# Performance work log

Hardware: AMD Instinct MI355X
Metric: run time of the kernel (lower is better)

## Reference

```python
import jax, jax.numpy as jnp
import numpy as np

N, E, D, G, S, H = 100000, 1600000, 64, 1024, 4096, 128
BN_EPS = 1e-5


def setup_inputs() -> dict:
    key = jax.random.key(0)
    ks = jax.random.split(key, 24)
    x = jax.random.normal(ks[0], (N, D), jnp.float32)
    sid = jax.random.randint(ks[1], (N,), 0, S)
    x = x.at[:, 5].set(sid.astype(jnp.float32))  # column 5 holds integer substructure ids
    edge_index = jax.random.randint(ks[2], (2, E), 0, N, dtype=jnp.int32)
    batch = jnp.sort(jax.random.randint(ks[3], (N,), 0, G, dtype=jnp.int32))

    def lin(k, fan_in, shape):
        return jax.random.normal(k, shape, jnp.float32) / np.sqrt(fan_in)

    return {
        "x": x, "edge_index": edge_index, "batch": batch,
        # substructure attention net: Linear(D,64) -> tanh -> Linear(64,1,no bias)
        "w1": lin(ks[4], D, (D, 64)), "b1": jnp.zeros((64,), jnp.float32),
        "w2": lin(ks[5], 64, (64,)),
        "cw0": lin(ks[6], D + 1, (D + 1, H)), "cb0": jnp.zeros((H,), jnp.float32),
        "cw_rest": lin(ks[7], H, (3, H, H)), "cb_rest": jnp.zeros((3, H), jnp.float32),
        # BatchNorm1d (eval mode: running stats)
        "bn_gamma": jnp.ones((4, H), jnp.float32), "bn_beta": jnp.zeros((4, H), jnp.float32),
        "bn_mean": 0.1 * jax.random.normal(ks[8], (4, H), jnp.float32),
        "bn_var": jax.random.uniform(ks[9], (4, H), jnp.float32, 0.5, 1.5),
        # pred head: Linear(128,64) -> ELU -> Linear(64,1)
        "hw1": lin(ks[10], H, (H, 64)), "hb1": jnp.zeros((64,), jnp.float32),
        "hw2": lin(ks[11], 64, (64, 1)), "hb2": jnp.zeros((1,), jnp.float32),
    }


def _subst_attention(x, subst_ids, w1, b1, w2):
    ones = jnp.ones((x.shape[0],), x.dtype)
    cnt = jax.ops.segment_sum(ones, subst_ids, num_segments=S)
    sums = jax.ops.segment_sum(x, subst_ids, num_segments=S)
    means = sums / jnp.maximum(cnt, 1.0)[:, None]          # [S, D] per-substructure mean
    scores = jnp.tanh(means @ w1 + b1) @ w2                # [S]
    attn = jax.nn.softmax(scores, axis=0)                  # softmax over substructures
    return attn[subst_ids][:, None]                        # [N, 1] broadcast back to atoms


def _gcn(x, W, b, row, col, norm, n):
    h = x @ W                                              # [N, H]
    msg = h[row] * norm[:, None]                           # gather + scale  [E+N, H]
    return jax.ops.segment_sum(msg, col, num_segments=n) + b


def reference(x, edge_index, batch, w1, b1, w2, cw0, cb0, cw_rest, cb_rest,
              bn_gamma, bn_beta, bn_mean, bn_var, hw1, hb1, hw2, hb2):
    n = x.shape[0]
    subst_ids = jax.lax.stop_gradient(x[:, 5]).astype(jnp.int32)
    attn = _subst_attention(x, subst_ids, w1, b1, w2)
    h = jnp.concatenate([x, attn], axis=1)                 # [N, D+1]

    # add self loops, symmetric GCN normalization (as in PyG GCNConv)
    loops = jnp.arange(n, dtype=edge_index.dtype)
    row = jnp.concatenate([edge_index[0], loops])
    col = jnp.concatenate([edge_index[1], loops])
    deg = jax.ops.segment_sum(jnp.ones_like(row, dtype=h.dtype), col, num_segments=n)
    dinv = jax.lax.rsqrt(jnp.maximum(deg, 1.0))
    norm = dinv[row] * dinv[col]

    def bn(z, i):
        return (z - bn_mean[i]) * jax.lax.rsqrt(bn_var[i] + BN_EPS) * bn_gamma[i] + bn_beta[i]

    h = jax.nn.elu(bn(_gcn(h, cw0, cb0, row, col, norm, n), 0))
    for i in range(3):
        z = bn(_gcn(h, cw_rest[i], cb_rest[i], row, col, norm, n), i + 1)
        h = jax.nn.elu(z) if i < 2 else jax.nn.relu(z)

    # global mean pool over graphs
    gcnt = jax.ops.segment_sum(jnp.ones((n,), h.dtype), batch, num_segments=G)
    pooled = jax.ops.segment_sum(h, batch, num_segments=G) / jnp.maximum(gcnt, 1.0)[:, None]

    return jax.nn.elu(pooled @ hw1 + hb1) @ hw2 + hb2      # [G, 1]
```

## Files before the change

kernel.cpp:

```cpp
#include <hip/hip_runtime.h>
#include <math.h>

static constexpr int SS = 4096;
static constexpr int HH = 128;
static constexpr float EPS_BN = 1e-5f;

typedef __attribute__((ext_vector_type(8))) short bf16x8;
typedef __attribute__((ext_vector_type(4))) float f32x4;

__device__ inline unsigned short f2bf(float f) {
  unsigned int u = __float_as_uint(f);
  return (unsigned short)((u + 0x7fffu + ((u >> 16) & 1u)) >> 16);
}
__device__ inline float bflo(unsigned int u) { return __uint_as_float(u << 16); }
__device__ inline float bfhi(unsigned int u) { return __uint_as_float(u & 0xffff0000u); }


__device__ void wpack_body(const float* __restrict__ W, unsigned short* __restrict__ out,
                           int nkc, int idx) {
  if (idx >= 8 * nkc * 64) return;
  int lane = idx & 63;
  int kc = (idx >> 6) % nkc;
  int nt = idx / (64 * nkc);
  int colc = nt * 16 + (lane & 15);
  int k0 = kc * 32 + (lane >> 4) * 8;
  unsigned int w[4];
  #pragma unroll
  for (int i = 0; i < 4; ++i) {
    unsigned short a = f2bf(W[(size_t)(k0 + 2 * i) * 128 + colc]);
    unsigned short b = f2bf(W[(size_t)(k0 + 2 * i + 1) * 128 + colc]);
    w[i] = (unsigned int)a | ((unsigned int)b << 16);
  }
  *(uint4*)&out[(size_t)idx * 8] = make_uint4(w[0], w[1], w[2], w[3]);
}

__global__ __launch_bounds__(256)
void gcn_front1(const int* __restrict__ col, int* __restrict__ fill, int* __restrict__ pos,
                const float* __restrict__ x, float* __restrict__ cnt, float* __restrict__ sums,
                unsigned int* __restrict__ xh, const int* __restrict__ batch,
                int* __restrict__ gstart,
                const float* __restrict__ cw0, const float* __restrict__ cwr,
                unsigned short* __restrict__ wpk0, unsigned short* __restrict__ wpkr,
                const float* __restrict__ cb0, const float* __restrict__ cbr,
                const float* __restrict__ bng, const float* __restrict__ bnb,
                const float* __restrict__ bnm, const float* __restrict__ bnv,
                float* __restrict__ bnS, float* __restrict__ bnT,
                int n, int e, int G,
                int nbPos, int nbSub, int nbXb, int nbGb, int nbW0, int nbWr) {
  int b = blockIdx.x;
  int t = threadIdx.x;
  if (b < nbPos) {
    int i = b * 256 + t;
    if (i < e) pos[i] = atomicAdd(&fill[col[i]], 1);
    return;
  }
  b -= nbPos;
  if (b < nbSub) {
    int node = b * 4 + (t >> 6);
    int lane = t & 63;
    if (node >= n) return;
    const float* xr = x + (size_t)node * 64;
    float v = xr[lane];
    int sid = (int)__shfl(v, 5, 64);
    if (lane == 0) atomicAdd(&cnt[sid], 1.0f);
    atomicAdd(&sums[(size_t)sid * 64 + lane], v);
    return;
  }
  b -= nbSub;
  if (b < nbXb) {
    int i = b * 256 + t;
    if (i >= n * 32) return;
    int pr = i & 31;
    float2 v = *(const float2*)&x[(size_t)(i >> 5) * 64 + pr * 2];
    if (pr == 2) v.y = 0.f;
    xh[i] = (unsigned int)f2bf(v.x) | ((unsigned int)f2bf(v.y) << 16);
    return;
  }
  b -= nbXb;
  if (b < nbGb) {
    int g = b * 256 + t;
    if (g > G) return;
    if (g == G) { gstart[G] = n; return; }
    int lo = 0, hi = n;
    while (lo < hi) { int mid = (lo + hi) >> 1; if (batch[mid] < g) lo = mid + 1; else hi = mid; }
    gstart[g] = lo;
    return;
  }
  b -= nbGb;
  if (b < nbW0) { wpack_body(cw0, wpk0, 2, b * 256 + t); return; }
  b -= nbW0;
  if (b < 3 * nbWr) {
    int l = b / nbWr, bb = b % nbWr;
    wpack_body(cwr + (size_t)l * HH * HH, wpkr + (size_t)l * 8 * 4 * 64 * 8, 4, bb * 256 + t);
    return;
  }
  b -= 3 * nbWr;
  {
    int i = b * 256 + t;
    if (i >= 512) return;
    int l = i >> 7, c = i & 127;
    float S = rsqrtf(bnv[i] + EPS_BN) * bng[i];
    float bias = (l == 0) ? cb0[c] : cbr[(l - 1) * 128 + c];
    bnS[i] = S;
    bnT[i] = fmaf(bias - bnm[i], S, bnb[i]);
  }
}


__global__ void gcn_scores(const float* __restrict__ sums, const float* __restrict__ cnt,
                           const float* __restrict__ w1, const float* __restrict__ b1,
                           const float* __restrict__ w2, float* __restrict__ scores) {
  int s = blockIdx.x * 4 + (threadIdx.x >> 6);
  int j = threadIdx.x & 63;
  float r = 1.0f / fmaxf(cnt[s], 1.0f);
  const float* ss = sums + (size_t)s * 64;
  float acc = b1[j];
  #pragma unroll 8
  for (int d = 0; d < 64; ++d) acc = fmaf(ss[d] * r, w1[d * 64 + j], acc);
  float t = tanhf(acc) * w2[j];
  #pragma unroll
  for (int off = 32; off; off >>= 1) t += __shfl_down(t, off, 64);
  if (j == 0) scores[s] = t;
}

__global__ void gcn_softmax(float* __restrict__ sc) {
  int t = threadIdx.x;
  int wid = t >> 6;
  float v[4]; float m = -INFINITY;
  for (int i = 0; i < 4; ++i) { v[i] = sc[t + i * 1024]; m = fmaxf(m, v[i]); }
  for (int off = 32; off; off >>= 1) m = fmaxf(m, __shfl_xor(m, off, 64));
  __shared__ float wmax[16];
  if ((t & 63) == 0) wmax[wid] = m;
  __syncthreads();
  if (t == 0) { float mm = wmax[0]; for (int i = 1; i < 16; ++i) mm = fmaxf(mm, wmax[i]); wmax[0] = mm; }
  __syncthreads();
  float M = wmax[0];
  float s = 0.f;
  for (int i = 0; i < 4; ++i) { v[i] = expf(v[i] - M); s += v[i]; }
  for (int off = 32; off; off >>= 1) s += __shfl_xor(s, off, 64);
  __shared__ float wsum[16];
  if ((t & 63) == 0) wsum[wid] = s;
  __syncthreads();
  if (t == 0) { float ts = 0.f; for (int i = 0; i < 16; ++i) ts += wsum[i]; wsum[0] = ts; }
  __syncthreads();
  float inv = 1.0f / wsum[0];
  for (int i = 0; i < 4; ++i) sc[t + i * 1024] = v[i] * inv;
}


__global__ void gcn_scan1(const int* __restrict__ fill, int* __restrict__ rowstart,
                          int* __restrict__ bsum, float* __restrict__ dinv, int n) {
  __shared__ int tmp[1024];
  int t = threadIdx.x; int g = blockIdx.x * 1024 + t;
  int v = (g < n) ? fill[g] : 0;
  if (g < n) dinv[g] = rsqrtf((float)v + 1.0f);
  tmp[t] = v; __syncthreads();
  for (int off = 1; off < 1024; off <<= 1) {
    int a = (t >= off) ? tmp[t - off] : 0; __syncthreads();
    tmp[t] += a; __syncthreads();
  }
  if (g < n) rowstart[g] = tmp[t] - v;
  if (t == 1023) bsum[blockIdx.x] = tmp[t];
}

__global__ void gcn_scan2(int* __restrict__ bsum, int nb) {
  __shared__ int tmp[128];
  int t = threadIdx.x;
  int v = (t < nb) ? bsum[t] : 0;
  tmp[t] = v; __syncthreads();
  for (int off = 1; off < 128; off <<= 1) {
    int a = (t >= off) ? tmp[t - off] : 0; __syncthreads();
    tmp[t] += a; __syncthreads();
  }
  if (t < nb) bsum[t] = tmp[t] - v;
}

__global__ void gcn_scan3(int* __restrict__ rowstart, const int* __restrict__ bsum, int n, int e) {
  int g = blockIdx.x * 1024 + threadIdx.x;
  if (g < n) rowstart[g] += bsum[blockIdx.x];
  if (g == 0) rowstart[n] = e;
}


__global__ __launch_bounds__(256)
void gcn_front3(const float* __restrict__ x, const float* __restrict__ attn,
                float2* __restrict__ np,
                const int* __restrict__ row, const int* __restrict__ col,
                const int* __restrict__ pos, const int* __restrict__ rowstart,
                const float* __restrict__ dinv, int2* __restrict__ sedge,
                int n, int e, int nbNp) {
  int b = blockIdx.x;
  int t = threadIdx.x;
  if (b < nbNp) {
    int i = b * 256 + t;
    if (i >= n) return;
    int sid = (int)x[(size_t)i * 64 + 5];
    np[i] = make_float2((float)sid, attn[sid]);
    return;
  }
  b -= nbNp;
  int i = b * 256 + t;
  if (i >= e) return;
  int c = col[i], r = row[i];
  sedge[rowstart[c] + pos[i]] = make_int2(r, __float_as_int(dinv[r] * dinv[c]));
}


__global__ __launch_bounds__(256)
void gcn_front4(const unsigned int* __restrict__ xh, const float2* __restrict__ np,
                const int2* __restrict__ sedge, const int* __restrict__ rowstart,
                const float* __restrict__ dinv,
                unsigned int* __restrict__ s0b, float* __restrict__ s0x,
                int n, int nbAx) {
  int blk = blockIdx.x;
  int t = threadIdx.x;
  if (blk < nbAx) {
    int node = blk * 4 + (t >> 6);
    int lane = t & 63;
    if (node >= n) return;
    int g = lane >> 3, sl = lane & 7;
    float di = dinv[node], d2 = di * di;
    const uint4* x4 = (const uint4*)xh;
    float a[8];
    if (g == 0) {
      uint4 u = x4[(size_t)node * 8 + sl];
      a[0] = bflo(u.x) * d2; a[1] = bfhi(u.x) * d2;
      a[2] = bflo(u.y) * d2; a[3] = bfhi(u.y) * d2;
      a[4] = bflo(u.z) * d2; a[5] = bfhi(u.z) * d2;
      a[6] = bflo(u.w) * d2; a[7] = bfhi(u.w) * d2;
    } else {
      #pragma unroll
      for (int i = 0; i < 8; ++i) a[i] = 0.f;
    }
    int s_ = rowstart[node], e_ = rowstart[node + 1];
    for (int b = s_; b < e_; b += 8) {
      int idx = b + (lane & 7);
      int2 se = (idx < e_) ? sedge[idx] : make_int2(node, 0);
      int src = __shfl(se.x, g, 8);
      float w = __int_as_float(__shfl(se.y, g, 8));
      uint4 u = x4[(size_t)src * 8 + sl];
      a[0] = fmaf(bflo(u.x), w, a[0]); a[1] = fmaf(bfhi(u.x), w, a[1]);
      a[2] = fmaf(bflo(u.y), w, a[2]); a[3] = fmaf(bfhi(u.y), w, a[3]);
      a[4] = fmaf(bflo(u.z), w, a[4]); a[5] = fmaf(bfhi(u.z), w, a[5]);
      a[6] = fmaf(bflo(u.w), w, a[6]); a[7] = fmaf(bfhi(u.w), w, a[7]);
    }
    #pragma unroll
    for (int i = 0; i < 8; ++i) {
      a[i] += __shfl_xor(a[i], 8, 64);
      a[i] += __shfl_xor(a[i], 16, 64);
      a[i] += __shfl_xor(a[i], 32, 64);
    }
    if (g == 0) {
      uint4 o;
      o.x = (unsigned)f2bf(a[0]) | ((unsigned)f2bf(a[1]) << 16);
      o.y = (unsigned)f2bf(a[2]) | ((unsigned)f2bf(a[3]) << 16);
      o.z = (unsigned)f2bf(a[4]) | ((unsigned)f2bf(a[5]) << 16);
      o.w = (unsigned)f2bf(a[6]) | ((unsigned)f2bf(a[7]) << 16);
      ((uint4*)s0b)[(size_t)node * 8 + sl] = o;
    }
    return;
  }
  int i = (blk - nbAx) * 256 + t;
  if (i >= n) return;
  float di = dinv[i], d2 = di * di;
  float2 self = np[i];
  float a5 = d2 * self.x, a64 = d2 * self.y;
  int s_ = rowstart[i], e_ = rowstart[i + 1];
  for (int ee = s_; ee < e_; ++ee) {
    int2 se = sedge[ee];
    float w = __int_as_float(se.y);
    float2 v = np[se.x];
    a5 = fmaf(v.x, w, a5);
    a64 = fmaf(v.y, w, a64);
  }
  s0x[(size_t)i * 2] = a5;
  s0x[(size_t)i * 2 + 1] = a64;
}


__global__ __launch_bounds__(256)
void gcn_aggB(const unsigned short* __restrict__ hB, const int2* __restrict__ sedge,
              const int* __restrict__ rowstart, const float* __restrict__ dinv,
              unsigned int* __restrict__ sBb, int n) {
  int node = blockIdx.x * 4 + (threadIdx.x >> 6);
  int lane = threadIdx.x & 63;
  if (node >= n) return;
  int g = lane >> 4, sl = lane & 15;
  float di = dinv[node], d2 = di * di;
  const uint4* h4 = (const uint4*)hB;
  float a[8];
  if (g == 0) {
    uint4 u = h4[(size_t)node * 16 + sl];
    a[0] = bflo(u.x) * d2; a[1] = bfhi(u.x) * d2;
    a[2] = bflo(u.y) * d2; a[3] = bfhi(u.y) * d2;
    a[4] = bflo(u.z) * d2; a[5] = bfhi(u.z) * d2;
    a[6] = bflo(u.w) * d2; a[7] = bfhi(u.w) * d2;
  } else {
    #pragma unroll
    for (int i = 0; i < 8; ++i) a[i] = 0.f;
  }
  int s_ = rowstart[node], e_ = rowstart[node + 1];
  for (int b = s_; b < e_; b += 8) {
    int idx = b + (lane & 7);
    int2 se = (idx < e_) ? sedge[idx] : make_int2(node, 0);
    #pragma unroll
    for (int j = 0; j < 2; ++j) {
      int src = __shfl(se.x, j * 4 + g, 8);
      float w = __int_as_float(__shfl(se.y, j * 4 + g, 8));
      uint4 u = h4[(size_t)src * 16 + sl];
      a[0] = fmaf(bflo(u.x), w, a[0]); a[1] = fmaf(bfhi(u.x), w, a[1]);
      a[2] = fmaf(bflo(u.y), w, a[2]); a[3] = fmaf(bfhi(u.y), w, a[3]);
      a[4] = fmaf(bflo(u.z), w, a[4]); a[5] = fmaf(bfhi(u.z), w, a[5]);
      a[6] = fmaf(bflo(u.w), w, a[6]); a[7] = fmaf(bfhi(u.w), w, a[7]);
    }
  }
  #pragma unroll
  for (int i = 0; i < 8; ++i) {
    a[i] += __shfl_xor(a[i], 16, 64);
    a[i] += __shfl_xor(a[i], 32, 64);
  }
  if (g == 0) {
    uint4 o;
    o.x = (unsigned)f2bf(a[0]) | ((unsigned)f2bf(a[1]) << 16);
    o.y = (unsigned)f2bf(a[2]) | ((unsigned)f2bf(a[3]) << 16);
    o.z = (unsigned)f2bf(a[4]) | ((unsigned)f2bf(a[5]) << 16);
    o.w = (unsigned)f2bf(a[6]) | ((unsigned)f2bf(a[7]) << 16);
    ((uint4*)sBb)[(size_t)node * 16 + sl] = o;
  }
}


__global__ __launch_bounds__(256)
void gcn_mm_mfma(const unsigned short* __restrict__ A, const unsigned short* __restrict__ Wpk,
                 const float* __restrict__ bnS, const float* __restrict__ bnT,
                 unsigned short* __restrict__ hB, int relu) {
  __shared__ unsigned short tile[4][16][136];
  int t = threadIdx.x;
  int wid = t >> 6, l = t & 63;
  int rowA = l & 15, kg = l >> 4;
  size_t row0w = (size_t)blockIdx.x * 64 + wid * 16;
  const unsigned short* Ar = A + (row0w + rowA) * 128 + kg * 8;
  bf16x8 af[4];
  #pragma unroll
  for (int kc = 0; kc < 4; ++kc) af[kc] = *(const bf16x8*)(Ar + kc * 32);
  f32x4 acc[8];
  #pragma unroll
  for (int nt = 0; nt < 8; ++nt) acc[nt] = (f32x4){0.f, 0.f, 0.f, 0.f};
  const unsigned short* wp = Wpk + (size_t)l * 8;
  #pragma unroll
  for (int kc = 0; kc < 4; ++kc) {
    bf16x8 bf[8];
    #pragma unroll
    for (int nt = 0; nt < 8; ++nt)
      bf[nt] = *(const bf16x8*)(wp + (size_t)(nt * 4 + kc) * 512);
    #pragma unroll
    for (int nt = 0; nt < 8; ++nt)
      acc[nt] = __builtin_amdgcn_mfma_f32_16x16x32_bf16(af[kc], bf[nt], acc[nt], 0, 0, 0);
  }
  int colb = l & 15, rb = kg * 4;
  #pragma unroll
  for (int nt = 0; nt < 8; ++nt) {
    int c = nt * 16 + colb;
    float S = bnS[c], T = bnT[c];
    #pragma unroll
    for (int j = 0; j < 4; ++j) {
      float v = fmaf(acc[nt][j], S, T);
      v = relu ? fmaxf(v, 0.f) : (v > 0.f ? v : expf(v) - 1.f);
      tile[wid][rb + j][c] = f2bf(v);
    }
  }
  __syncthreads();
  #pragma unroll
  for (int i = 0; i < 4; ++i) {
    int m = i * 64 + l;
    int row = m >> 4, chunk = m & 15;
    uint4 v = *(const uint4*)&tile[wid][row][chunk * 8];
    *(uint4*)&hB[(row0w + row) * 128 + chunk * 8] = v;
  }
}

__global__ __launch_bounds__(256)
void gcn_mm0_mfma(const unsigned short* __restrict__ A, const float* __restrict__ s0x,
                  const unsigned short* __restrict__ Wpk0, const float* __restrict__ cw0,
                  const float* __restrict__ bnS, const float* __restrict__ bnT,
                  unsigned short* __restrict__ hB) {
  __shared__ unsigned short tile[4][16][136];
  int t = threadIdx.x;
  int wid = t >> 6, l = t & 63;
  int rowA = l & 15, kg = l >> 4;
  size_t row0w = (size_t)blockIdx.x * 64 + wid * 16;
  const unsigned short* Ar = A + (row0w + rowA) * 64 + kg * 8;
  bf16x8 af[2];
  #pragma unroll
  for (int kc = 0; kc < 2; ++kc) af[kc] = *(const bf16x8*)(Ar + kc * 32);
  f32x4 acc[8];
  #pragma unroll
  for (int nt = 0; nt < 8; ++nt) acc[nt] = (f32x4){0.f, 0.f, 0.f, 0.f};
  const unsigned short* wp = Wpk0 + (size_t)l * 8;
  #pragma unroll
  for (int kc = 0; kc < 2; ++kc) {
    bf16x8 bf[8];
    #pragma unroll
    for (int nt = 0; nt < 8; ++nt)
      bf[nt] = *(const bf16x8*)(wp + (size_t)(nt * 2 + kc) * 512);
    #pragma unroll
    for (int nt = 0; nt < 8; ++nt)
      acc[nt] = __builtin_amdgcn_mfma_f32_16x16x32_bf16(af[kc], bf[nt], acc[nt], 0, 0, 0);
  }
  int colb = l & 15, rb = kg * 4;
  float2 ax[4];
  #pragma unroll
  for (int j = 0; j < 4; ++j) ax[j] = *(const float2*)&s0x[(row0w + rb + j) * 2];
  #pragma unroll
  for (int nt = 0; nt < 8; ++nt) {
    int c = nt * 16 + colb;
    float w5 = cw0[5 * 128 + c], w64 = cw0[64 * 128 + c];
    float S = bnS[c], T = bnT[c];
    #pragma unroll
    for (int j = 0; j < 4; ++j) {
      float z = acc[nt][j] + ax[j].x * w5 + ax[j].y * w64;
      float v = fmaf(z, S, T);
      v = v > 0.f ? v : expf(v) - 1.f;
      tile[wid][rb + j][c] = f2bf(v);
    }
  }
  __syncthreads();
  #pragma unroll
  for (int i = 0; i < 4; ++i) {
    int m = i * 64 + l;
    int row = m >> 4, chunk = m & 15;
    uint4 v = *(const uint4*)&tile[wid][row][chunk * 8];
    *(uint4*)&hB[(row0w + row) * 128 + chunk * 8] = v;
  }
}


__global__ void gcn_pool2(const unsigned short* __restrict__ hB, const int* __restrict__ gstart,
                          float* __restrict__ pooled, int G) {
  int g = blockIdx.x * 4 + (threadIdx.x >> 6);
  int lane = threadIdx.x & 63;
  if (g >= G) return;
  int s = gstart[g], epos = gstart[g + 1];
  const unsigned int* h32 = (const unsigned int*)hB;
  float ax = 0.f, ay = 0.f;
  for (int i = s; i < epos; ++i) {
    unsigned int u = h32[(size_t)i * 64 + lane];
    ax += bflo(u);
    ay += bfhi(u);
  }
  float r = 1.0f / fmaxf((float)(epos - s), 1.0f);
  ((float2*)pooled)[(size_t)g * 64 + lane] = make_float2(ax * r, ay * r);
}

__global__ void gcn_head(const float* __restrict__ pooled,
                         const float* __restrict__ hw1, const float* __restrict__ hb1,
                         const float* __restrict__ hw2, const float* __restrict__ hb2,
                         float* __restrict__ out, int g) {
  int gi = blockIdx.x * 4 + (threadIdx.x >> 6);
  int j = threadIdx.x & 63;
  if (gi >= g) return;
  const float* p = pooled + (size_t)gi * 128;
  float acc = hb1[j];
  #pragma unroll 8
  for (int k = 0; k < 128; ++k) acc = fmaf(p[k], hw1[k * 64 + j], acc);
  float t = acc > 0.f ? acc : expf(acc) - 1.f;
  t *= hw2[j];
  #pragma unroll
  for (int off = 32; off; off >>= 1) t += __shfl_down(t, off, 64);
  if (j == 0) out[gi] = t + hb2[0];
}


extern "C" void kernel_launch(void* const* d_in, const int* in_sizes, int n_in,
                              void* d_out, int out_size, void* d_ws, size_t ws_size,
                              hipStream_t stream) {
  const float* x   = (const float*)d_in[0];
  const int*   ei  = (const int*)d_in[1];
  const int*   batch = (const int*)d_in[2];
  const float* w1  = (const float*)d_in[3];
  const float* b1  = (const float*)d_in[4];
  const float* w2  = (const float*)d_in[5];
  const float* cw0 = (const float*)d_in[6];
  const float* cb0 = (const float*)d_in[7];
  const float* cwr = (const float*)d_in[8];
  const float* cbr = (const float*)d_in[9];
  const float* bng = (const float*)d_in[10];
  const float* bnb = (const float*)d_in[11];
  const float* bnm = (const float*)d_in[12];
  const float* bnv = (const float*)d_in[13];
  const float* hw1 = (const float*)d_in[14];
  const float* hb1 = (const float*)d_in[15];
  const float* hw2 = (const float*)d_in[16];
  const float* hb2 = (const float*)d_in[17];
  float* out = (float*)d_out;
  (void)n_in; (void)ws_size;

  const int n = in_sizes[0] / 64;
  const int e = in_sizes[1] / 2;
  const int G = out_size;
  const int* row = ei;
  const int* col = ei + e;
  const int nb128 = (n + 127) / 128;
  const int n_pad = nb128 * 128;

  char* p = (char*)d_ws;
  auto take = [&](size_t bytes) { char* r = p; p += (bytes + 255) & ~(size_t)255; return r; };
  float* cnt    = (float*)take((size_t)SS * 4);
  float* sums   = (float*)take((size_t)SS * 64 * 4);
  float* attn   = (float*)take((size_t)SS * 4);
  float* dinv   = (float*)take((size_t)n * 4);
  int*   rowst  = (int*)take(((size_t)n + 1) * 4);
  int*   fill   = (int*)take((size_t)n * 4);
  int*   pos    = (int*)take((size_t)e * 4);
  int*   bsum   = (int*)take(128 * 4);
  int*   gstart = (int*)take(((size_t)G + 1) * 4);
  int2*  sedge  = (int2*)take((size_t)e * 8);
  float* pooled = (float*)take((size_t)G * HH * 4);
  float2* np    = (float2*)take((size_t)n * 8);
  unsigned int* xh = (unsigned int*)take((size_t)n * 32 * 4);
  unsigned int* s0b = (unsigned int*)take((size_t)n_pad * 32 * 4);
  float* s0x    = (float*)take((size_t)n_pad * 2 * 4);
  unsigned int* sBb = (unsigned int*)take((size_t)n_pad * 64 * 4);
  unsigned short* hB = (unsigned short*)take((size_t)n_pad * HH * 2);
  unsigned short* wpk0 = (unsigned short*)take((size_t)8 * 2 * 64 * 8 * 2);
  unsigned short* wpkr = (unsigned short*)take((size_t)3 * 8 * 4 * 64 * 8 * 2);
  float* bnS    = (float*)take(4 * 128 * 4);
  float* bnT    = (float*)take(4 * 128 * 4);

  hipMemsetAsync(cnt, 0, (size_t)SS * 4, stream);
  hipMemsetAsync(sums, 0, (size_t)SS * 64 * 4, stream);
  hipMemsetAsync(fill, 0, (size_t)n * 4, stream);

  int nbPos = (e + 255) / 256;
  int nbSub = (n + 3) / 4;
  int nbXb  = (n * 32 + 255) / 256;
  int nbGb  = (G + 1 + 255) / 256;
  int nbW0 = 4, nbWr = 8, nbBnp = 2;
  int front1 = nbPos + nbSub + nbXb + nbGb + nbW0 + 3 * nbWr + nbBnp;
  gcn_front1<<<front1, 256, 0, stream>>>(col, fill, pos, x, cnt, sums, xh, batch, gstart,
      cw0, cwr, wpk0, wpkr, cb0, cbr, bng, bnb, bnm, bnv, bnS, bnT,
      n, e, G, nbPos, nbSub, nbXb, nbGb, nbW0, nbWr);

  gcn_scores<<<SS / 4, 256, 0, stream>>>(sums, cnt, w1, b1, w2, attn);
  gcn_softmax<<<1, 1024, 0, stream>>>(attn);

  int nb = (n + 1023) / 1024;
  gcn_scan1<<<nb, 1024, 0, stream>>>(fill, rowst, bsum, dinv, n);
  gcn_scan2<<<1, 128, 0, stream>>>(bsum, nb);
  gcn_scan3<<<nb, 1024, 0, stream>>>(rowst, bsum, n, e);

  int nbNp = (n + 255) / 256, nbSc = (e + 255) / 256;
  gcn_front3<<<nbNp + nbSc, 256, 0, stream>>>(x, attn, np, row, col, pos, rowst, dinv,
      sedge, n, e, nbNp);

  int nbAx = (n + 3) / 4, nbAnp = (n + 255) / 256;
  gcn_front4<<<nbAx + nbAnp, 256, 0, stream>>>(xh, np, sedge, rowst, dinv, s0b, s0x, n, nbAx);
  gcn_mm0_mfma<<<n_pad / 64, 256, 0, stream>>>((const unsigned short*)s0b, s0x, wpk0, cw0,
      bnS, bnT, hB);

  for (int l = 0; l < 3; ++l) {
    gcn_aggB<<<(n + 3) / 4, 256, 0, stream>>>(hB, sedge, rowst, dinv, sBb, n);
    gcn_mm_mfma<<<n_pad / 64, 256, 0, stream>>>((const unsigned short*)sBb,
        wpkr + (size_t)l * 8 * 4 * 64 * 8, bnS + (l + 1) * 128, bnT + (l + 1) * 128,
        hB, l == 2 ? 1 : 0);
  }

  gcn_pool2<<<(G + 3) / 4, 256, 0, stream>>>(hB, gstart, pooled, G);
  gcn_head<<<(G + 3) / 4, 256, 0, stream>>>(pooled, hw1, hb1, hw2, hb2, out, G);
}
```

Baseline: 634.6 us.

## Fuse neighbor aggregation into MFMA matmul kernels for each GCN layer

```diff
diff --git a/kernel.cpp b/kernel.cpp
--- a/kernel.cpp
+++ b/kernel.cpp
@@ -207,142 +207,56 @@
 
 
 __global__ __launch_bounds__(256)
-void gcn_front4(const unsigned int* __restrict__ xh, const float2* __restrict__ np,
-                const int2* __restrict__ sedge, const int* __restrict__ rowstart,
-                const float* __restrict__ dinv,
-                unsigned int* __restrict__ s0b, float* __restrict__ s0x,
-                int n, int nbAx) {
-  int blk = blockIdx.x;
-  int t = threadIdx.x;
-  if (blk < nbAx) {
-    int node = blk * 4 + (t >> 6);
-    int lane = t & 63;
-    if (node >= n) return;
-    int g = lane >> 3, sl = lane & 7;
-    float di = dinv[node], d2 = di * di;
-    const uint4* x4 = (const uint4*)xh;
-    float a[8];
-    if (g == 0) {
-      uint4 u = x4[(size_t)node * 8 + sl];
-      a[0] = bflo(u.x) * d2; a[1] = bfhi(u.x) * d2;
-      a[2] = bflo(u.y) * d2; a[3] = bfhi(u.y) * d2;
-      a[4] = bflo(u.z) * d2; a[5] = bfhi(u.z) * d2;
-      a[6] = bflo(u.w) * d2; a[7] = bfhi(u.w) * d2;
-    } else {
-      #pragma unroll
-      for (int i = 0; i < 8; ++i) a[i] = 0.f;
-    }
-    int s_ = rowstart[node], e_ = rowstart[node + 1];
-    for (int b = s_; b < e_; b += 8) {
-      int idx = b + (lane & 7);
-      int2 se = (idx < e_) ? sedge[idx] : make_int2(node, 0);
-      int src = __shfl(se.x, g, 8);
-      float w = __int_as_float(__shfl(se.y, g, 8));
-      uint4 u = x4[(size_t)src * 8 + sl];
-      a[0] = fmaf(bflo(u.x), w, a[0]); a[1] = fmaf(bfhi(u.x), w, a[1]);
-      a[2] = fmaf(bflo(u.y), w, a[2]); a[3] = fmaf(bfhi(u.y), w, a[3]);
-      a[4] = fmaf(bflo(u.z), w, a[4]); a[5] = fmaf(bfhi(u.z), w, a[5]);
-      a[6] = fmaf(bflo(u.w), w, a[6]); a[7] = fmaf(bfhi(u.w), w, a[7]);
-    }
-    #pragma unroll
-    for (int i = 0; i < 8; ++i) {
-      a[i] += __shfl_xor(a[i], 8, 64);
-      a[i] += __shfl_xor(a[i], 16, 64);
-      a[i] += __shfl_xor(a[i], 32, 64);
-    }
-    if (g == 0) {
-      uint4 o;
-      o.x = (unsigned)f2bf(a[0]) | ((unsigned)f2bf(a[1]) << 16);
-      o.y = (unsigned)f2bf(a[2]) | ((unsigned)f2bf(a[3]) << 16);
-      o.z = (unsigned)f2bf(a[4]) | ((unsigned)f2bf(a[5]) << 16);
-      o.w = (unsigned)f2bf(a[6]) | ((unsigned)f2bf(a[7]) << 16);
-      ((uint4*)s0b)[(size_t)node * 8 + sl] = o;
-    }
-    return;
-  }
-  int i = (blk - nbAx) * 256 + t;
-  if (i >= n) return;
-  float di = dinv[i], d2 = di * di;
-  float2 self = np[i];
-  float a5 = d2 * self.x, a64 = d2 * self.y;
-  int s_ = rowstart[i], e_ = rowstart[i + 1];
-  for (int ee = s_; ee < e_; ++ee) {
-    int2 se = sedge[ee];
-    float w = __int_as_float(se.y);
-    float2 v = np[se.x];
-    a5 = fmaf(v.x, w, a5);
-    a64 = fmaf(v.y, w, a64);
-  }
-  s0x[(size_t)i * 2] = a5;
-  s0x[(size_t)i * 2 + 1] = a64;
-}
-
-
-__global__ __launch_bounds__(256)
-void gcn_aggB(const unsigned short* __restrict__ hB, const int2* __restrict__ sedge,
-              const int* __restrict__ rowstart, const float* __restrict__ dinv,
-              unsigned int* __restrict__ sBb, int n) {
-  int node = blockIdx.x * 4 + (threadIdx.x >> 6);
-  int lane = threadIdx.x & 63;
-  if (node >= n) return;
-  int g = lane >> 4, sl = lane & 15;
-  float di = dinv[node], d2 = di * di;
-  const uint4* h4 = (const uint4*)hB;
-  float a[8];
-  if (g == 0) {
-    uint4 u = h4[(size_t)node * 16 + sl];
-    a[0] = bflo(u.x) * d2; a[1] = bfhi(u.x) * d2;
-    a[2] = bflo(u.y) * d2; a[3] = bfhi(u.y) * d2;
-    a[4] = bflo(u.z) * d2; a[5] = bfhi(u.z) * d2;
-    a[6] = bflo(u.w) * d2; a[7] = bfhi(u.w) * d2;
-  } else {
-    #pragma unroll
-    for (int i = 0; i < 8; ++i) a[i] = 0.f;
-  }
-  int s_ = rowstart[node], e_ = rowstart[node + 1];
-  for (int b = s_; b < e_; b += 8) {
-    int idx = b + (lane & 7);
-    int2 se = (idx < e_) ? sedge[idx] : make_int2(node, 0);
-    #pragma unroll
-    for (int j = 0; j < 2; ++j) {
-      int src = __shfl(se.x, j * 4 + g, 8);
-      float w = __int_as_float(__shfl(se.y, j * 4 + g, 8));
-      uint4 u = h4[(size_t)src * 16 + sl];
-      a[0] = fmaf(bflo(u.x), w, a[0]); a[1] = fmaf(bfhi(u.x), w, a[1]);
-      a[2] = fmaf(bflo(u.y), w, a[2]); a[3] = fmaf(bfhi(u.y), w, a[3]);
-      a[4] = fmaf(bflo(u.z), w, a[4]); a[5] = fmaf(bfhi(u.z), w, a[5]);
-      a[6] = fmaf(bflo(u.w), w, a[6]); a[7] = fmaf(bfhi(u.w), w, a[7]);
-    }
-  }
-  #pragma unroll
-  for (int i = 0; i < 8; ++i) {
-    a[i] += __shfl_xor(a[i], 16, 64);
-    a[i] += __shfl_xor(a[i], 32, 64);
-  }
-  if (g == 0) {
-    uint4 o;
-    o.x = (unsigned)f2bf(a[0]) | ((unsigned)f2bf(a[1]) << 16);
-    o.y = (unsigned)f2bf(a[2]) | ((unsigned)f2bf(a[3]) << 16);
-    o.z = (unsigned)f2bf(a[4]) | ((unsigned)f2bf(a[5]) << 16);
-    o.w = (unsigned)f2bf(a[6]) | ((unsigned)f2bf(a[7]) << 16);
-    ((uint4*)sBb)[(size_t)node * 16 + sl] = o;
-  }
-}
-
-
-__global__ __launch_bounds__(256)
-void gcn_mm_mfma(const unsigned short* __restrict__ A, const unsigned short* __restrict__ Wpk,
+void gcn_layer_f(const unsigned short* __restrict__ hIn, const int2* __restrict__ sedge,
+                 const int* __restrict__ rowstart, const float* __restrict__ dinv,
+                 const unsigned short* __restrict__ Wpk,
                  const float* __restrict__ bnS, const float* __restrict__ bnT,
-                 unsigned short* __restrict__ hB, int relu) {
+                 unsigned short* __restrict__ hOut, int relu, int n) {
   __shared__ unsigned short tile[4][16][136];
   int t = threadIdx.x;
   int wid = t >> 6, l = t & 63;
-  int rowA = l & 15, kg = l >> 4;
+  int r = l & 15, kg = l >> 4;
   size_t row0w = (size_t)blockIdx.x * 64 + wid * 16;
-  const unsigned short* Ar = A + (row0w + rowA) * 128 + kg * 8;
+  int noderaw = (int)row0w + r;
+  bool valid = noderaw < n;
+  int node = valid ? noderaw : n - 1;
+  float di = dinv[node], d2 = di * di;
+  const uint4* h4 = (const uint4*)hIn;
+  float a[4][8];
+  #pragma unroll
+  for (int kc = 0; kc < 4; ++kc) {
+    uint4 u = h4[(size_t)node * 16 + kc * 4 + kg];
+    a[kc][0] = bflo(u.x) * d2; a[kc][1] = bfhi(u.x) * d2;
+    a[kc][2] = bflo(u.y) * d2; a[kc][3] = bfhi(u.y) * d2;
+    a[kc][4] = bflo(u.z) * d2; a[kc][5] = bfhi(u.z) * d2;
+    a[kc][6] = bflo(u.w) * d2; a[kc][7] = bfhi(u.w) * d2;
+  }
+  int s_ = valid ? rowstart[node] : 0;
+  int e_ = valid ? rowstart[node + 1] : 0;
+  int2 se = (s_ < e_) ? sedge[s_] : make_int2(0, 0);
+  for (int j = s_; j < e_; ++j) {
+    int2 cur = se;
+    if (j + 1 < e_) se = sedge[j + 1];
+    float w = __int_as_float(cur.y);
+    #pragma unroll
+    for (int kc = 0; kc < 4; ++kc) {
+      uint4 u = h4[(size_t)cur.x * 16 + kc * 4 + kg];
+      a[kc][0] = fmaf(bflo(u.x), w, a[kc][0]); a[kc][1] = fmaf(bfhi(u.x), w, a[kc][1]);
+      a[kc][2] = fmaf(bflo(u.y), w, a[kc][2]); a[kc][3] = fmaf(bfhi(u.y), w, a[kc][3]);
+      a[kc][4] = fmaf(bflo(u.z), w, a[kc][4]); a[kc][5] = fmaf(bfhi(u.z), w, a[kc][5]);
+      a[kc][6] = fmaf(bflo(u.w), w, a[kc][6]); a[kc][7] = fmaf(bfhi(u.w), w, a[kc][7]);
+    }
+  }
   bf16x8 af[4];
   #pragma unroll
-  for (int kc = 0; kc < 4; ++kc) af[kc] = *(const bf16x8*)(Ar + kc * 32);
+  for (int kc = 0; kc < 4; ++kc) {
+    uint4 pk;
+    pk.x = (unsigned)f2bf(a[kc][0]) | ((unsigned)f2bf(a[kc][1]) << 16);
+    pk.y = (unsigned)f2bf(a[kc][2]) | ((unsigned)f2bf(a[kc][3]) << 16);
+    pk.z = (unsigned)f2bf(a[kc][4]) | ((unsigned)f2bf(a[kc][5]) << 16);
+    pk.w = (unsigned)f2bf(a[kc][6]) | ((unsigned)f2bf(a[kc][7]) << 16);
+    af[kc] = *(bf16x8*)&pk;
+  }
   f32x4 acc[8];
   #pragma unroll
   for (int nt = 0; nt < 8; ++nt) acc[nt] = (f32x4){0.f, 0.f, 0.f, 0.f};
@@ -373,26 +287,72 @@
   #pragma unroll
   for (int i = 0; i < 4; ++i) {
     int m = i * 64 + l;
-    int row = m >> 4, chunk = m & 15;
-    uint4 v = *(const uint4*)&tile[wid][row][chunk * 8];
-    *(uint4*)&hB[(row0w + row) * 128 + chunk * 8] = v;
-  }
-}
+    int rr = m >> 4, chunk = m & 15;
+    uint4 v = *(const uint4*)&tile[wid][rr][chunk * 8];
+    *(uint4*)&hOut[(row0w + rr) * 128 + chunk * 8] = v;
+  }
+}
+
 
 __global__ __launch_bounds__(256)
-void gcn_mm0_mfma(const unsigned short* __restrict__ A, const float* __restrict__ s0x,
-                  const unsigned short* __restrict__ Wpk0, const float* __restrict__ cw0,
+void gcn_layer0_f(const unsigned int* __restrict__ xh, const float2* __restrict__ np,
+                  const int2* __restrict__ sedge, const int* __restrict__ rowstart,
+                  const float* __restrict__ dinv, const unsigned short* __restrict__ Wpk0,
+                  const float* __restrict__ cw0,
                   const float* __restrict__ bnS, const float* __restrict__ bnT,
-                  unsigned short* __restrict__ hB) {
+                  unsigned short* __restrict__ hOut, int n) {
   __shared__ unsigned short tile[4][16][136];
   int t = threadIdx.x;
   int wid = t >> 6, l = t & 63;
-  int rowA = l & 15, kg = l >> 4;
+  int r = l & 15, kg = l >> 4;
   size_t row0w = (size_t)blockIdx.x * 64 + wid * 16;
-  const unsigned short* Ar = A + (row0w + rowA) * 64 + kg * 8;
+  int noderaw = (int)row0w + r;
+  bool valid = noderaw < n;
+  int node = valid ? noderaw : n - 1;
+  float di = dinv[node], d2 = di * di;
+  const uint4* x4 = (const uint4*)xh;
+  float a[2][8];
+  #pragma unroll
+  for (int kc = 0; kc < 2; ++kc) {
+    uint4 u = x4[(size_t)node * 8 + kc * 4 + kg];
+    a[kc][0] = bflo(u.x) * d2; a[kc][1] = bfhi(u.x) * d2;
+    a[kc][2] = bflo(u.y) * d2; a[kc][3] = bfhi(u.y) * d2;
+    a[kc][4] = bflo(u.z) * d2; a[kc][5] = bfhi(u.z) * d2;
+    a[kc][6] = bflo(u.w) * d2; a[kc][7] = bfhi(u.w) * d2;
+  }
+  float a5 = 0.f, a64 = 0.f;
+  if (kg == 0) { float2 v = np[node]; a5 = d2 * v.x; a64 = d2 * v.y; }
+  int s_ = valid ? rowstart[node] : 0;
+  int e_ = valid ? rowstart[node + 1] : 0;
+  int2 se = (s_ < e_) ? sedge[s_] : make_int2(0, 0);
+  for (int j = s_; j < e_; ++j) {
+    int2 cur = se;
+    if (j + 1 < e_) se = sedge[j + 1];
+    float w = __int_as_float(cur.y);
+    #pragma unroll
+    for (int kc = 0; kc < 2; ++kc) {
+      uint4 u = x4[(size_t)cur.x * 8 + kc * 4 + kg];
+      a[kc][0] = fmaf(bflo(u.x), w, a[kc][0]); a[kc][1] = fmaf(bfhi(u.x), w, a[kc][1]);
+      a[kc][2] = fmaf(bflo(u.y), w, a[kc][2]); a[kc][3] = fmaf(bfhi(u.y), w, a[kc][3]);
+      a[kc][4] = fmaf(bflo(u.z), w, a[kc][4]); a[kc][5] = fmaf(bfhi(u.z), w, a[kc][5]);
+      a[kc][6] = fmaf(bflo(u.w), w, a[kc][6]); a[kc][7] = fmaf(bfhi(u.w), w, a[kc][7]);
+    }
+    if (kg == 0) {
+      float2 v = np[cur.x];
+      a5 = fmaf(v.x, w, a5);
+      a64 = fmaf(v.y, w, a64);
+    }
+  }
   bf16x8 af[2];
   #pragma unroll
-  for (int kc = 0; kc < 2; ++kc) af[kc] = *(const bf16x8*)(Ar + kc * 32);
+  for (int kc = 0; kc < 2; ++kc) {
+    uint4 pk;
+    pk.x = (unsigned)f2bf(a[kc][0]) | ((unsigned)f2bf(a[kc][1]) << 16);
+    pk.y = (unsigned)f2bf(a[kc][2]) | ((unsigned)f2bf(a[kc][3]) << 16);
+    pk.z = (unsigned)f2bf(a[kc][4]) | ((unsigned)f2bf(a[kc][5]) << 16);
+    pk.w = (unsigned)f2bf(a[kc][6]) | ((unsigned)f2bf(a[kc][7]) << 16);
+    af[kc] = *(bf16x8*)&pk;
+  }
   f32x4 acc[8];
   #pragma unroll
   for (int nt = 0; nt < 8; ++nt) acc[nt] = (f32x4){0.f, 0.f, 0.f, 0.f};
@@ -410,7 +370,10 @@
   int colb = l & 15, rb = kg * 4;
   float2 ax[4];
   #pragma unroll
-  for (int j = 0; j < 4; ++j) ax[j] = *(const float2*)&s0x[(row0w + rb + j) * 2];
+  for (int j = 0; j < 4; ++j) {
+    ax[j].x = __shfl(a5, rb + j, 64);
+    ax[j].y = __shfl(a64, rb + j, 64);
+  }
   #pragma unroll
   for (int nt = 0; nt < 8; ++nt) {
     int c = nt * 16 + colb;
@@ -428,9 +391,9 @@
   #pragma unroll
   for (int i = 0; i < 4; ++i) {
     int m = i * 64 + l;
-    int row = m >> 4, chunk = m & 15;
-    uint4 v = *(const uint4*)&tile[wid][row][chunk * 8];
-    *(uint4*)&hB[(row0w + row) * 128 + chunk * 8] = v;
+    int rr = m >> 4, chunk = m & 15;
+    uint4 v = *(const uint4*)&tile[wid][rr][chunk * 8];
+    *(uint4*)&hOut[(row0w + rr) * 128 + chunk * 8] = v;
   }
 }
 
@@ -518,10 +481,8 @@
   float* pooled = (float*)take((size_t)G * HH * 4);
   float2* np    = (float2*)take((size_t)n * 8);
   unsigned int* xh = (unsigned int*)take((size_t)n * 32 * 4);
-  unsigned int* s0b = (unsigned int*)take((size_t)n_pad * 32 * 4);
-  float* s0x    = (float*)take((size_t)n_pad * 2 * 4);
-  unsigned int* sBb = (unsigned int*)take((size_t)n_pad * 64 * 4);
-  unsigned short* hB = (unsigned short*)take((size_t)n_pad * HH * 2);
+  unsigned short* hP0 = (unsigned short*)take((size_t)n_pad * HH * 2);
+  unsigned short* hP1 = (unsigned short*)take((size_t)n_pad * HH * 2);
   unsigned short* wpk0 = (unsigned short*)take((size_t)8 * 2 * 64 * 8 * 2);
   unsigned short* wpkr = (unsigned short*)take((size_t)3 * 8 * 4 * 64 * 8 * 2);
   float* bnS    = (float*)take(4 * 128 * 4);
@@ -553,18 +514,15 @@
   gcn_front3<<<nbNp + nbSc, 256, 0, stream>>>(x, attn, np, row, col, pos, rowst, dinv,
       sedge, n, e, nbNp);
 
-  int nbAx = (n + 3) / 4, nbAnp = (n + 255) / 256;
-  gcn_front4<<<nbAx + nbAnp, 256, 0, stream>>>(xh, np, sedge, rowst, dinv, s0b, s0x, n, nbAx);
-  gcn_mm0_mfma<<<n_pad / 64, 256, 0, stream>>>((const unsigned short*)s0b, s0x, wpk0, cw0,
-      bnS, bnT, hB);
-
-  for (int l = 0; l < 3; ++l) {
-    gcn_aggB<<<(n + 3) / 4, 256, 0, stream>>>(hB, sedge, rowst, dinv, sBb, n);
-    gcn_mm_mfma<<<n_pad / 64, 256, 0, stream>>>((const unsigned short*)sBb,
-        wpkr + (size_t)l * 8 * 4 * 64 * 8, bnS + (l + 1) * 128, bnT + (l + 1) * 128,
-        hB, l == 2 ? 1 : 0);
-  }
-
-  gcn_pool2<<<(G + 3) / 4, 256, 0, stream>>>(hB, gstart, pooled, G);
+  gcn_layer0_f<<<n_pad / 64, 256, 0, stream>>>(xh, np, sedge, rowst, dinv, wpk0, cw0,
+      bnS, bnT, hP0, n);
+  gcn_layer_f<<<n_pad / 64, 256, 0, stream>>>(hP0, sedge, rowst, dinv, wpkr,
+      bnS + 128, bnT + 128, hP1, 0, n);
+  gcn_layer_f<<<n_pad / 64, 256, 0, stream>>>(hP1, sedge, rowst, dinv,
+      wpkr + (size_t)8 * 4 * 64 * 8, bnS + 256, bnT + 256, hP0, 0, n);
+  gcn_layer_f<<<n_pad / 64, 256, 0, stream>>>(hP0, sedge, rowst, dinv,
+      wpkr + (size_t)2 * 8 * 4 * 64 * 8, bnS + 384, bnT + 384, hP1, 1, n);
+
+  gcn_pool2<<<(G + 3) / 4, 256, 0, stream>>>(hP1, gstart, pooled, G);
   gcn_head<<<(G + 3) / 4, 256, 0, stream>>>(pooled, hw1, hb1, hw2, hb2, out, G);
 }
```

Measured after the change: 625.4 us. No clear change (-1.5%).
